# Kernel tuning notes

Measured on AMD Instinct MI355X. Metric: run time of the kernel, lower is better.

## Reference

```python
import jax, jax.numpy as jnp
import numpy as np
import math

D_MODEL = 1024
NHEAD = 16
HEAD_DIM = D_MODEL // NHEAD  # 64
FREQ = 10000.0


def _rope(x, freq=FREQ):
    # x: [B, H, S, D] with D even. Matches RotaryEmbedding.apply:
    # thetas = exp(-2*log(freq)*(i//2)/D) for i in [0, D/2)
    S, D = x.shape[-2], x.shape[-1]
    pos = jnp.arange(S, dtype=x.dtype)                       # [S]
    idx = jnp.arange(D // 2) // 2                            # floor(i/2)
    thetas = jnp.exp((-2.0 * math.log(freq) / D) * idx.astype(x.dtype))  # [D/2]
    ang = pos[:, None] * thetas[None, :]                     # [S, D/2]
    cos, sin = jnp.cos(ang), jnp.sin(ang)
    x2 = x.reshape(*x.shape[:-1], D // 2, 2)
    x0, x1 = x2[..., 0], x2[..., 1]
    out = jnp.stack([x0 * cos - x1 * sin, x0 * sin + x1 * cos], axis=-1)
    return out.reshape(x.shape)


def setup_inputs() -> dict:
    key = jax.random.key(0)
    k1, k2, k3, k4, k5 = jax.random.split(key, 5)
    B, S = 2, 2048
    scale = 1.0 / math.sqrt(D_MODEL)
    return {
        "embeddings": jax.random.normal(k1, (B, S, D_MODEL), dtype=jnp.float32),
        "W_qkv": jax.random.normal(k2, (D_MODEL, 3 * D_MODEL), dtype=jnp.float32) * scale,
        "b_qkv": jnp.zeros((3 * D_MODEL,), dtype=jnp.float32),
        "W_o": jax.random.normal(k4, (D_MODEL, D_MODEL), dtype=jnp.float32) * scale,
        "b_o": jnp.zeros((D_MODEL,), dtype=jnp.float32),
    }


def reference(embeddings, W_qkv, b_qkv, W_o, b_o):
    B, S, _ = embeddings.shape
    qkv = embeddings @ W_qkv + b_qkv                          # [B,S,3*D]
    q, k, v = jnp.split(qkv, 3, axis=-1)

    def split_heads(t):  # [B,S,D] -> [B,H,S,hd]
        return t.reshape(B, S, NHEAD, HEAD_DIM).transpose(0, 2, 1, 3)

    q, k, v = split_heads(q), split_heads(k), split_heads(v)
    q = _rope(q)
    k = _rope(k)

    scores = jnp.einsum("bhqd,bhkd->bhqk", q, k) / math.sqrt(HEAD_DIM)
    attn = jax.nn.softmax(scores, axis=-1)
    heads = jnp.einsum("bhqk,bhkd->bhqd", attn, v)            # [B,H,S,hd]
    out = heads.transpose(0, 2, 1, 3).reshape(B, S, D_MODEL)
    return out @ W_o + b_o
```

## Files before the change

kernel.cpp:

```cpp
#include <hip/hip_runtime.h>
#include <hip/hip_bf16.h>
#include <math.h>

typedef __bf16 bf16;
typedef __bf16 bf16x4 __attribute__((ext_vector_type(4)));
typedef __bf16 bf16x8 __attribute__((ext_vector_type(8)));
typedef float f32x4 __attribute__((ext_vector_type(4)));

#define DEV static __device__ __forceinline__

#define SS 2048
#define HH 16
#define HD 64

DEV void load_lds16(const bf16* g, bf16* l) {
  __builtin_amdgcn_global_load_lds(
      (const __attribute__((address_space(1))) unsigned int*)g,
      (__attribute__((address_space(3))) unsigned int*)l, 16, 0, 0);
}

__global__ __launch_bounds__(256) void k_prep(
    const float* __restrict__ emb, bf16* __restrict__ Xb,
    const float* __restrict__ Wqkv, bf16* __restrict__ Wqt,
    const float* __restrict__ Wo, bf16* __restrict__ Wot) {
  __shared__ float tt[32][33];
  int bid = blockIdx.x;
  if (bid < 4096) {
    int i = (bid * 256 + threadIdx.x) * 4;
    float4 v = *reinterpret_cast<const float4*>(emb + i);
    bf16x4 o = {(bf16)v.x, (bf16)v.y, (bf16)v.z, (bf16)v.w};
    *reinterpret_cast<bf16x4*>(Xb + i) = o;
    return;
  }
  const float* in;
  bf16* out;
  int R = 1024, C, ctile, rtile;
  if (bid < 7168) {
    in = Wqkv; out = Wqt; C = 3072;
    int idx = bid - 4096; ctile = idx % 96; rtile = idx / 96;
  } else {
    in = Wo; out = Wot; C = 1024;
    int idx = bid - 7168; ctile = idx & 31; rtile = idx >> 5;
  }
  int tx = threadIdx.x & 31, ty = threadIdx.x >> 5;
#pragma unroll
  for (int i = 0; i < 4; ++i)
    tt[ty + 8 * i][tx] = in[(rtile * 32 + ty + 8 * i) * C + ctile * 32 + tx];
  __syncthreads();
#pragma unroll
  for (int i = 0; i < 4; ++i) {
    int oc = ctile * 32 + ty + 8 * i;
    out[oc * R + rtile * 32 + tx] = (bf16)tt[tx][ty + 8 * i];
  }
}

DEV void gemm_core(const bf16* __restrict__ Ab, const bf16* __restrict__ Bb,
                   bf16* As, bf16* Bs, int w, int l, f32x4 acc[4][4]) {
  int fr = l & 15, fg = l >> 4;
  int wr = (w >> 1) * 64, wc = (w & 1) * 64;
  for (int kt = 0; kt < 16; ++kt) {
#pragma unroll
    for (int i = 0; i < 4; ++i) {
      int blk = w * 4 + i;
      const bf16* ga = Ab + (blk * 8 + (l >> 3)) * 1024 + kt * 64 + (l & 7) * 8;
      const bf16* gb = Bb + (blk * 8 + (l >> 3)) * 1024 + kt * 64 + (l & 7) * 8;
      load_lds16(ga, As + blk * 512);
      load_lds16(gb, Bs + blk * 512);
    }
    __syncthreads();
#pragma unroll
    for (int kk = 0; kk < 2; ++kk) {
      bf16x8 af[4], bfv[4];
#pragma unroll
      for (int mi = 0; mi < 4; ++mi)
        af[mi] = *(const bf16x8*)(As + (wr + mi * 16 + fr) * 64 + kk * 32 + fg * 8);
#pragma unroll
      for (int ni = 0; ni < 4; ++ni)
        bfv[ni] = *(const bf16x8*)(Bs + (wc + ni * 16 + fr) * 64 + kk * 32 + fg * 8);
#pragma unroll
      for (int mi = 0; mi < 4; ++mi)
#pragma unroll
        for (int ni = 0; ni < 4; ++ni)
          acc[mi][ni] = __builtin_amdgcn_mfma_f32_16x16x32_bf16(
              af[mi], bfv[ni], acc[mi][ni], 0, 0, 0);
    }
    __syncthreads();
  }
}

__global__ __launch_bounds__(256) void k_gemm1(
    const bf16* __restrict__ A, const bf16* __restrict__ Bt,
    const float* __restrict__ bias, bf16* __restrict__ Qo,
    bf16* __restrict__ Ko, bf16* __restrict__ Vo) {
  __shared__ bf16 As[128 * 64], Bs[128 * 64];
  int wg = blockIdx.x;
  int bm = wg & 31, bn = wg >> 5;
  int t = threadIdx.x, w = t >> 6, l = t & 63;
  f32x4 acc[4][4];
#pragma unroll
  for (int mi = 0; mi < 4; ++mi)
#pragma unroll
    for (int ni = 0; ni < 4; ++ni) acc[mi][ni] = (f32x4){0.f, 0.f, 0.f, 0.f};
  gemm_core(A + bm * 128 * 1024, Bt + bn * 128 * 1024, As, Bs, w, l, acc);
  int fr = l & 15, fg = l >> 4;
  int wr = (w >> 1) * 64, wc = (w & 1) * 64;
#pragma unroll
  for (int mi = 0; mi < 4; ++mi)
#pragma unroll
    for (int ni = 0; ni < 4; ++ni) {
      int gc = bn * 128 + wc + ni * 16 + fr;
      int sec = gc >> 10, cc = gc & 1023;
      bf16* dst = sec == 0 ? Qo : (sec == 1 ? Ko : Vo);
      int h = cc >> 6, d = cc & 63;
      float bb = bias[gc];
      int gr0 = bm * 128 + wr + mi * 16 + fg * 4;
#pragma unroll
      for (int r = 0; r < 4; ++r) {
        int gr = gr0 + r;
        int b = gr >> 11, s = gr & 2047;
        dst[((b * HH + h) * SS + s) * HD + d] = (bf16)(acc[mi][ni][r] + bb);
      }
    }
}

__global__ __launch_bounds__(256) void k_gemm2(
    const bf16* __restrict__ A, const bf16* __restrict__ Bt,
    const float* __restrict__ bias, float* __restrict__ out) {
  __shared__ bf16 As[128 * 64], Bs[128 * 64];
  int wg = blockIdx.x;
  int bm = wg & 31, bn = wg >> 5;
  int t = threadIdx.x, w = t >> 6, l = t & 63;
  f32x4 acc[4][4];
#pragma unroll
  for (int mi = 0; mi < 4; ++mi)
#pragma unroll
    for (int ni = 0; ni < 4; ++ni) acc[mi][ni] = (f32x4){0.f, 0.f, 0.f, 0.f};
  gemm_core(A + bm * 128 * 1024, Bt + bn * 128 * 1024, As, Bs, w, l, acc);
  int fr = l & 15, fg = l >> 4;
  int wr = (w >> 1) * 64, wc = (w & 1) * 64;
#pragma unroll
  for (int mi = 0; mi < 4; ++mi)
#pragma unroll
    for (int ni = 0; ni < 4; ++ni) {
      int gc = bn * 128 + wc + ni * 16 + fr;
      float bb = bias[gc];
      int gr0 = bm * 128 + wr + mi * 16 + fg * 4;
#pragma unroll
      for (int r = 0; r < 4; ++r)
        out[(gr0 + r) * 1024 + gc] = acc[mi][ni][r] + bb;
    }
}

__global__ void k_rope(bf16* __restrict__ Qb, bf16* __restrict__ Kb) {
  int t = blockIdx.x * 256 + threadIdx.x;
  bf16* buf = (t >> 19) ? Kb : Qb;
  float qs = (t >> 19) ? 1.0f : 0.125f;
  int g = t & 524287;
  int j = g & 7;
  int s = (g >> 3) & 2047;
  bf16* p = buf + (long long)g * 8;
  const float CN = -0.28782313662425572f;
  float th0 = __expf(CN * (float)(2 * j));
  float th1 = __expf(CN * (float)(2 * j + 1));
  float sp = (float)s;
  float s0, c0, s1, c1;
  sincosf(sp * th0, &s0, &c0);
  sincosf(sp * th1, &s1, &c1);
  bf16x8 v = *(bf16x8*)p;
  float x[8];
#pragma unroll
  for (int i = 0; i < 8; ++i) x[i] = (float)v[i];
  float o[8];
  o[0] = x[0] * c0 - x[1] * s0; o[1] = x[0] * s0 + x[1] * c0;
  o[2] = x[2] * c0 - x[3] * s0; o[3] = x[2] * s0 + x[3] * c0;
  o[4] = x[4] * c1 - x[5] * s1; o[5] = x[4] * s1 + x[5] * c1;
  o[6] = x[6] * c1 - x[7] * s1; o[7] = x[6] * s1 + x[7] * c1;
  bf16x8 ov;
#pragma unroll
  for (int i = 0; i < 8; ++i) ov[i] = (bf16)(o[i] * qs);
  *(bf16x8*)p = ov;
}

__global__ void k_trV(const bf16* __restrict__ V, bf16* __restrict__ Vt) {
  __shared__ bf16 t[64][66];
  int st = blockIdx.x, bh = blockIdx.y;
  const bf16* vb = V + (long long)bh * SS * HD;
  bf16* ob = Vt + (long long)bh * HD * SS;
  int tx = threadIdx.x & 63, ty = threadIdx.x >> 6;
#pragma unroll
  for (int i = 0; i < 16; ++i)
    t[ty + 4 * i][tx] = vb[(st * 64 + ty + 4 * i) * 64 + tx];
  __syncthreads();
#pragma unroll
  for (int i = 0; i < 16; ++i) {
    int dR = ty + 4 * i;
    ob[dR * SS + st * 64 + tx] = t[tx][dR];
  }
}

#define MFMA(a, b, c) __builtin_amdgcn_mfma_f32_16x16x32_bf16(a, b, c, 0, 0, 0)

__global__ __launch_bounds__(512) void k_attn(
    const bf16* __restrict__ Q, const bf16* __restrict__ K,
    const bf16* __restrict__ Vt, bf16* __restrict__ Hd) {
  __shared__ bf16 KVs[2][8192];
  __shared__ bf16 plds[8][16][72];
  int bid = blockIdx.x;
  int x = bid & 7, rr = bid >> 3;
  int bh = x * 4 + (rr & 3);
  int qt = rr >> 2;
  int b = bh >> 4, h = bh & 15;
  int t = threadIdx.x, w = t >> 6, l = t & 63;
  int fr = l & 15, fg = l >> 4;
  const bf16* Qb = Q + (long long)bh * SS * HD;
  const bf16* Kb = K + (long long)bh * SS * HD;
  const bf16* Vb = Vt + (long long)bh * HD * SS;
  bool isK = w < 4;
  int stride = isK ? 64 : 2048;
  int wrow = (isK ? w : (w - 4)) * 16 + (l >> 3);
  const bf16* src = (isK ? Kb : Vb) + wrow * stride + ((l & 7) ^ (l >> 3)) * 8;
  int adv = isK ? 4096 : 64;
  int dbase = w * 1024;

  int q0 = qt * 128 + w * 16;
  bf16x8 qf0 = *(const bf16x8*)(Qb + (q0 + fr) * 64 + fg * 8);
  bf16x8 qf1 = *(const bf16x8*)(Qb + (q0 + fr) * 64 + 32 + fg * 8);
  f32x4 acc[4];
#pragma unroll
  for (int db = 0; db < 4; ++db) acc[db] = (f32x4){0.f, 0.f, 0.f, 0.f};
  float ssum = 0.f;
  const f32x4 zero = {0.f, 0.f, 0.f, 0.f};
  int xo = fr & 7;

  load_lds16(src, &KVs[0][dbase]);
  load_lds16(src + 8 * stride, &KVs[0][dbase + 512]);
  src += adv;
  __syncthreads();

  for (int it = 0; it < 32; ++it) {
    int buf = it & 1;
    if (it < 31) {
      load_lds16(src, &KVs[buf ^ 1][dbase]);
      load_lds16(src + 8 * stride, &KVs[buf ^ 1][dbase + 512]);
      src += adv;
    }
    const bf16* Ks = &KVs[buf][0];
    const bf16* Vs = &KVs[buf][4096];
    f32x4 stl[4];
    __builtin_amdgcn_s_setprio(1);
#pragma unroll
    for (int ks = 0; ks < 4; ++ks) {
      bf16x8 k0 = *(const bf16x8*)(Ks + (ks * 16 + fr) * 64 + (fg ^ xo) * 8);
      bf16x8 k1 = *(const bf16x8*)(Ks + (ks * 16 + fr) * 64 + ((4 + fg) ^ xo) * 8);
      stl[ks] = MFMA(k0, qf0, zero);
      stl[ks] = MFMA(k1, qf1, stl[ks]);
    }
    __builtin_amdgcn_s_setprio(0);
    float ps = 0.f;
#pragma unroll
    for (int ks = 0; ks < 4; ++ks) {
      bf16x4 pb;
#pragma unroll
      for (int r = 0; r < 4; ++r) {
        float p = __expf(stl[ks][r] - 16.0f);
        ps += p;
        pb[r] = (bf16)p;
      }
      *(bf16x4*)&plds[w][fr][ks * 16 + fg * 4] = pb;
    }
    ssum += ps;
    bf16x8 pf0 = *(const bf16x8*)&plds[w][fr][fg * 8];
    bf16x8 pf1 = *(const bf16x8*)&plds[w][fr][32 + fg * 8];
    __builtin_amdgcn_s_setprio(1);
#pragma unroll
    for (int db = 0; db < 4; ++db) {
      bf16x8 vf0 = *(const bf16x8*)(Vs + (db * 16 + fr) * 64 + (fg ^ xo) * 8);
      bf16x8 vf1 = *(const bf16x8*)(Vs + (db * 16 + fr) * 64 + ((4 + fg) ^ xo) * 8);
      acc[db] = MFMA(vf0, pf0, acc[db]);
      acc[db] = MFMA(vf1, pf1, acc[db]);
    }
    __builtin_amdgcn_s_setprio(0);
    __syncthreads();
  }
  float sv = ssum;
  sv += __shfl_xor(sv, 16);
  sv += __shfl_xor(sv, 32);
  float inv = 1.0f / sv;
  int s = q0 + fr;
#pragma unroll
  for (int db = 0; db < 4; ++db) {
    bf16x4 ob;
#pragma unroll
    for (int r = 0; r < 4; ++r) ob[r] = (bf16)(acc[db][r] * inv);
    *(bf16x4*)(Hd + ((long long)(b * SS + s)) * 1024 + h * 64 + db * 16 + fg * 4) = ob;
  }
}

extern "C" void kernel_launch(void* const* d_in, const int* in_sizes, int n_in,
                              void* d_out, int out_size, void* d_ws, size_t ws_size,
                              hipStream_t stream) {
  const float* emb = (const float*)d_in[0];
  const float* Wqkv = (const float*)d_in[1];
  const float* bqkv = (const float*)d_in[2];
  const float* Wo = (const float*)d_in[3];
  const float* bo = (const float*)d_in[4];
  float* out = (float*)d_out;
  char* ws = (char*)d_ws;
  bf16* Xb  = (bf16*)(ws);
  bf16* Wqt = (bf16*)(ws + 8388608);
  bf16* Wot = (bf16*)(ws + 14680064);
  bf16* Qb  = (bf16*)(ws + 16777216);
  bf16* Kb  = (bf16*)(ws + 25165824);
  bf16* Vb  = (bf16*)(ws + 33554432);
  bf16* Vt  = (bf16*)(ws + 41943040);
  bf16* Hd  = (bf16*)(ws + 50331648);

  hipLaunchKernelGGL(k_prep, dim3(8192), dim3(256), 0, stream, emb, Xb, Wqkv, Wqt, Wo, Wot);
  hipLaunchKernelGGL(k_gemm1, dim3(768), dim3(256), 0, stream, Xb, Wqt, bqkv, Qb, Kb, Vb);
  hipLaunchKernelGGL(k_rope, dim3(4096), dim3(256), 0, stream, Qb, Kb);
  hipLaunchKernelGGL(k_trV, dim3(32, 32), dim3(256), 0, stream, Vb, Vt);
  hipLaunchKernelGGL(k_attn, dim3(512), dim3(512), 0, stream, Qb, Kb, Vt, Hd);
  hipLaunchKernelGGL(k_gemm2, dim3(256), dim3(256), 0, stream, Hd, Wot, bo, out);
}
```

Baseline: 143.8 us.

## Rewrite QKV GEMM with 256x256 tiles, double-buffered LDS, and swizzle

The QKV projection GEMM now uses 256x256 output tiles with 512 threads (8 waves, each computing 128x64), so the grid shrinks from 768 to 192 workgroups. Global-to-LDS loads for the next k-tile are issued in chunks between MFMA groups into a double buffer, which leaves one barrier per iteration. The LDS layout uses an XOR swizzle to avoid bank conflicts, MFMA sections are wrapped in s_setprio, and workgroups are remapped across XCDs for cache locality. The intent is more operand reuse and overlap of loads with compute. In exchange it uses 128KB of LDS and many accumulator registers, and with only 192 workgroups it runs one wave of workgroups on fewer CUs than the GPU has.

Result: faster. 138.4 us (-3.7%).

```diff
diff --git a/kernel.cpp b/kernel.cpp
--- a/kernel.cpp
+++ b/kernel.cpp
@@ -18,6 +18,8 @@
       (const __attribute__((address_space(1))) unsigned int*)g,
       (__attribute__((address_space(3))) unsigned int*)l, 16, 0, 0);
 }
+
+#define MFMA(a, b, c) __builtin_amdgcn_mfma_f32_16x16x32_bf16(a, b, c, 0, 0, 0)
 
 __global__ __launch_bounds__(256) void k_prep(
     const float* __restrict__ emb, bf16* __restrict__ Xb,
@@ -54,6 +56,128 @@
   }
 }
 
+__global__ __launch_bounds__(512) void k_gemm1(
+    const bf16* __restrict__ A, const bf16* __restrict__ Bt,
+    const float* __restrict__ bias, bf16* __restrict__ Qo,
+    bf16* __restrict__ Ko, bf16* __restrict__ Vo) {
+  __shared__ bf16 As[2][16384];
+  __shared__ bf16 Bs[2][16384];
+  int wg = blockIdx.x;
+  int xcd = wg & 7, idx = wg >> 3;
+  int wgid = xcd * 24 + idx;
+  int bm = wgid & 15, bn = wgid >> 4;
+  int t = threadIdx.x, w = t >> 6, l = t & 63;
+  int wm = w >> 2, wn = w & 3;
+  int fr = l & 15, fg = l >> 4;
+  const bf16* Ab = A + bm * 256 * 1024;
+  const bf16* Bb = Bt + bn * 256 * 1024;
+  int trow = t >> 3;
+  const bf16* sA = Ab + trow * 1024 + (((t & 7) ^ (trow & 7)) * 8);
+  const bf16* sB = Bb + trow * 1024 + (((t & 7) ^ (trow & 7)) * 8);
+  int dst0 = (w << 9);
+#pragma unroll
+  for (int j = 0; j < 4; ++j) {
+    load_lds16(sA + j * 65536, &As[0][j * 4096 + dst0]);
+    load_lds16(sB + j * 65536, &Bs[0][j * 4096 + dst0]);
+  }
+  f32x4 acc[8][4];
+#pragma unroll
+  for (int mi = 0; mi < 8; ++mi)
+#pragma unroll
+    for (int ni = 0; ni < 4; ++ni) acc[mi][ni] = (f32x4){0.f, 0.f, 0.f, 0.f};
+  int xo = fr & 7;
+  __syncthreads();
+  for (int kt = 0; kt < 16; ++kt) {
+    const bf16* Asb = &As[kt & 1][0];
+    const bf16* Bsb = &Bs[kt & 1][0];
+    bf16* An = &As[(kt & 1) ^ 1][0];
+    bf16* Bn = &Bs[(kt & 1) ^ 1][0];
+    bool st = kt < 15;
+    int ko = (kt + 1) * 64;
+    bf16x8 av[4], bv[4];
+    if (st) {
+      load_lds16(sA + ko, &An[dst0]);
+      load_lds16(sA + 65536 + ko, &An[4096 + dst0]);
+    }
+#pragma unroll
+    for (int ni = 0; ni < 4; ++ni)
+      bv[ni] = *(const bf16x8*)(Bsb + (wn * 64 + ni * 16 + fr) * 64 + (fg ^ xo) * 8);
+#pragma unroll
+    for (int mi = 0; mi < 4; ++mi)
+      av[mi] = *(const bf16x8*)(Asb + (wm * 128 + mi * 16 + fr) * 64 + (fg ^ xo) * 8);
+    __builtin_amdgcn_s_setprio(1);
+#pragma unroll
+    for (int mi = 0; mi < 4; ++mi)
+#pragma unroll
+      for (int ni = 0; ni < 4; ++ni)
+        acc[mi][ni] = MFMA(av[mi], bv[ni], acc[mi][ni]);
+    __builtin_amdgcn_s_setprio(0);
+    if (st) {
+      load_lds16(sA + 131072 + ko, &An[8192 + dst0]);
+      load_lds16(sA + 196608 + ko, &An[12288 + dst0]);
+    }
+#pragma unroll
+    for (int mi = 0; mi < 4; ++mi)
+      av[mi] = *(const bf16x8*)(Asb + (wm * 128 + (mi + 4) * 16 + fr) * 64 + (fg ^ xo) * 8);
+    __builtin_amdgcn_s_setprio(1);
+#pragma unroll
+    for (int mi = 0; mi < 4; ++mi)
+#pragma unroll
+      for (int ni = 0; ni < 4; ++ni)
+        acc[mi + 4][ni] = MFMA(av[mi], bv[ni], acc[mi + 4][ni]);
+    __builtin_amdgcn_s_setprio(0);
+    if (st) {
+      load_lds16(sB + ko, &Bn[dst0]);
+      load_lds16(sB + 65536 + ko, &Bn[4096 + dst0]);
+    }
+#pragma unroll
+    for (int ni = 0; ni < 4; ++ni)
+      bv[ni] = *(const bf16x8*)(Bsb + (wn * 64 + ni * 16 + fr) * 64 + ((4 + fg) ^ xo) * 8);
+#pragma unroll
+    for (int mi = 0; mi < 4; ++mi)
+      av[mi] = *(const bf16x8*)(Asb + (wm * 128 + mi * 16 + fr) * 64 + ((4 + fg) ^ xo) * 8);
+    __builtin_amdgcn_s_setprio(1);
+#pragma unroll
+    for (int mi = 0; mi < 4; ++mi)
+#pragma unroll
+      for (int ni = 0; ni < 4; ++ni)
+        acc[mi][ni] = MFMA(av[mi], bv[ni], acc[mi][ni]);
+    __builtin_amdgcn_s_setprio(0);
+    if (st) {
+      load_lds16(sB + 131072 + ko, &Bn[8192 + dst0]);
+      load_lds16(sB + 196608 + ko, &Bn[12288 + dst0]);
+    }
+#pragma unroll
+    for (int mi = 0; mi < 4; ++mi)
+      av[mi] = *(const bf16x8*)(Asb + (wm * 128 + (mi + 4) * 16 + fr) * 64 + ((4 + fg) ^ xo) * 8);
+    __builtin_amdgcn_s_setprio(1);
+#pragma unroll
+    for (int mi = 0; mi < 4; ++mi)
+#pragma unroll
+      for (int ni = 0; ni < 4; ++ni)
+        acc[mi + 4][ni] = MFMA(av[mi], bv[ni], acc[mi + 4][ni]);
+    __builtin_amdgcn_s_setprio(0);
+    __syncthreads();
+  }
+#pragma unroll
+  for (int mi = 0; mi < 8; ++mi)
+#pragma unroll
+    for (int ni = 0; ni < 4; ++ni) {
+      int gc = bn * 256 + wn * 64 + ni * 16 + fr;
+      int sec = gc >> 10, cc = gc & 1023;
+      bf16* dst = sec == 0 ? Qo : (sec == 1 ? Ko : Vo);
+      int h = cc >> 6, d = cc & 63;
+      float bb = bias[gc];
+      int gr0 = bm * 256 + wm * 128 + mi * 16 + fg * 4;
+#pragma unroll
+      for (int r = 0; r < 4; ++r) {
+        int gr = gr0 + r;
+        int b = gr >> 11, s = gr & 2047;
+        dst[((b * HH + h) * SS + s) * HD + d] = (bf16)(acc[mi][ni][r] + bb);
+      }
+    }
+}
+
 DEV void gemm_core(const bf16* __restrict__ Ab, const bf16* __restrict__ Bb,
                    bf16* As, bf16* Bs, int w, int l, f32x4 acc[4][4]) {
   int fr = l & 15, fg = l >> 4;
@@ -86,41 +210,6 @@
     }
     __syncthreads();
   }
-}
-
-__global__ __launch_bounds__(256) void k_gemm1(
-    const bf16* __restrict__ A, const bf16* __restrict__ Bt,
-    const float* __restrict__ bias, bf16* __restrict__ Qo,
-    bf16* __restrict__ Ko, bf16* __restrict__ Vo) {
-  __shared__ bf16 As[128 * 64], Bs[128 * 64];
-  int wg = blockIdx.x;
-  int bm = wg & 31, bn = wg >> 5;
-  int t = threadIdx.x, w = t >> 6, l = t & 63;
-  f32x4 acc[4][4];
-#pragma unroll
-  for (int mi = 0; mi < 4; ++mi)
-#pragma unroll
-    for (int ni = 0; ni < 4; ++ni) acc[mi][ni] = (f32x4){0.f, 0.f, 0.f, 0.f};
-  gemm_core(A + bm * 128 * 1024, Bt + bn * 128 * 1024, As, Bs, w, l, acc);
-  int fr = l & 15, fg = l >> 4;
-  int wr = (w >> 1) * 64, wc = (w & 1) * 64;
-#pragma unroll
-  for (int mi = 0; mi < 4; ++mi)
-#pragma unroll
-    for (int ni = 0; ni < 4; ++ni) {
-      int gc = bn * 128 + wc + ni * 16 + fr;
-      int sec = gc >> 10, cc = gc & 1023;
-      bf16* dst = sec == 0 ? Qo : (sec == 1 ? Ko : Vo);
-      int h = cc >> 6, d = cc & 63;
-      float bb = bias[gc];
-      int gr0 = bm * 128 + wr + mi * 16 + fg * 4;
-#pragma unroll
-      for (int r = 0; r < 4; ++r) {
-        int gr = gr0 + r;
-        int b = gr >> 11, s = gr & 2047;
-        dst[((b * HH + h) * SS + s) * HD + d] = (bf16)(acc[mi][ni][r] + bb);
-      }
-    }
 }
 
 __global__ __launch_bounds__(256) void k_gemm2(
@@ -197,8 +286,6 @@
     ob[dR * SS + st * 64 + tx] = t[tx][dR];
   }
 }
-
-#define MFMA(a, b, c) __builtin_amdgcn_mfma_f32_16x16x32_bf16(a, b, c, 0, 0, 0)
 
 __global__ __launch_bounds__(512) void k_attn(
     const bf16* __restrict__ Q, const bf16* __restrict__ K,
@@ -316,7 +403,7 @@
   bf16* Hd  = (bf16*)(ws + 50331648);
 
   hipLaunchKernelGGL(k_prep, dim3(8192), dim3(256), 0, stream, emb, Xb, Wqkv, Wqt, Wo, Wot);
-  hipLaunchKernelGGL(k_gemm1, dim3(768), dim3(256), 0, stream, Xb, Wqt, bqkv, Qb, Kb, Vb);
+  hipLaunchKernelGGL(k_gemm1, dim3(192), dim3(512), 0, stream, Xb, Wqt, bqkv, Qb, Kb, Vb);
   hipLaunchKernelGGL(k_rope, dim3(4096), dim3(256), 0, stream, Qb, Kb);
   hipLaunchKernelGGL(k_trV, dim3(32, 32), dim3(256), 0, stream, Vb, Vt);
   hipLaunchKernelGGL(k_attn, dim3(512), dim3(512), 0, stream, Qb, Kb, Vt, Hd);
```

## Rewrite QKV GEMM with 256x256 tiles, double-buffered LDS, XOR swizzle

Applied to the files above, without the earlier changes.

Replaces the 128x128 QKV projection GEMM with a 512-thread 256x256 tile kernel. It double-buffers LDS so global-to-LDS loads overlap the MFMA work, XOR-swizzles LDS to avoid bank conflicts, sets wave priority around the MFMA blocks, and remaps block indices so each XCD handles a group of neighbouring tiles. The larger tile raises operand reuse, but the grid shrinks to 192 blocks on a 256-CU device, which leaves some CUs idle and raises register pressure from 32 accumulators per lane.

New measurement: 132.8 us. 7.6% less time.

```diff
diff --git a/kernel.cpp b/kernel.cpp
--- a/kernel.cpp
+++ b/kernel.cpp
@@ -18,6 +18,8 @@
       (const __attribute__((address_space(1))) unsigned int*)g,
       (__attribute__((address_space(3))) unsigned int*)l, 16, 0, 0);
 }
+
+#define MFMA(a, b, c) __builtin_amdgcn_mfma_f32_16x16x32_bf16(a, b, c, 0, 0, 0)
 
 __global__ __launch_bounds__(256) void k_prep(
     const float* __restrict__ emb, bf16* __restrict__ Xb,
@@ -54,6 +56,106 @@
   }
 }
 
+__global__ __launch_bounds__(512) void k_gemm1(
+    const bf16* __restrict__ A, const bf16* __restrict__ Bt,
+    const float* __restrict__ bias, bf16* __restrict__ Qo,
+    bf16* __restrict__ Ko, bf16* __restrict__ Vo) {
+  __shared__ bf16 As[2][16384];
+  __shared__ bf16 Bs[2][16384];
+  int wg = blockIdx.x;
+  int xcd = wg & 7, idx = wg >> 3;
+  int bm = (xcd & 3) * 4 + (idx & 3);
+  int bn = (xcd >> 2) * 6 + (idx >> 2);
+  int t = threadIdx.x, w = t >> 6, l = t & 63;
+  int wm = w >> 2, wn = w & 3;
+  int fr = l & 15, fg = l >> 4;
+  const bf16* Ab = A + bm * 256 * 1024;
+  const bf16* Bb = Bt + bn * 256 * 1024;
+  int trow = t >> 3;
+  const bf16* sA = Ab + trow * 1024 + (((t & 7) ^ (trow & 7)) * 8);
+  const bf16* sB = Bb + trow * 1024 + (((t & 7) ^ (trow & 7)) * 8);
+  int dst0 = (w << 9);
+  int xo = fr & 7;
+
+#define G1_STAGE(buf, ko)                                         \
+  do {                                                            \
+    _Pragma("unroll")                                             \
+    for (int j = 0; j < 4; ++j) {                                 \
+      load_lds16(sA + j * 65536 + (ko), &As[buf][j * 4096 + dst0]); \
+      load_lds16(sB + j * 65536 + (ko), &Bs[buf][j * 4096 + dst0]); \
+    }                                                             \
+  } while (0)
+
+  f32x4 acc[8][4];
+#pragma unroll
+  for (int mi = 0; mi < 8; ++mi)
+#pragma unroll
+    for (int ni = 0; ni < 4; ++ni) acc[mi][ni] = (f32x4){0.f, 0.f, 0.f, 0.f};
+
+  G1_STAGE(0, 0);
+  asm volatile("s_waitcnt vmcnt(0)" ::: "memory");
+  __builtin_amdgcn_s_barrier();
+
+  for (int kt = 0; kt < 16; ++kt) {
+    int p = kt & 1;
+    const bf16* Asb = &As[p][0];
+    const bf16* Bsb = &Bs[p][0];
+    if (kt < 15) G1_STAGE(p ^ 1, (kt + 1) * 64);
+    bf16x8 av[8], bv[4];
+#pragma unroll
+    for (int ni = 0; ni < 4; ++ni)
+      bv[ni] = *(const bf16x8*)(Bsb + (wn * 64 + ni * 16 + fr) * 64 + (fg ^ xo) * 8);
+#pragma unroll
+    for (int mi = 0; mi < 8; ++mi)
+      av[mi] = *(const bf16x8*)(Asb + (wm * 128 + mi * 16 + fr) * 64 + (fg ^ xo) * 8);
+    asm volatile("s_waitcnt lgkmcnt(0)" ::: "memory");
+    __builtin_amdgcn_sched_barrier(0);
+    __builtin_amdgcn_s_setprio(1);
+#pragma unroll
+    for (int mi = 0; mi < 8; ++mi)
+#pragma unroll
+      for (int ni = 0; ni < 4; ++ni)
+        acc[mi][ni] = MFMA(av[mi], bv[ni], acc[mi][ni]);
+    __builtin_amdgcn_s_setprio(0);
+#pragma unroll
+    for (int ni = 0; ni < 4; ++ni)
+      bv[ni] = *(const bf16x8*)(Bsb + (wn * 64 + ni * 16 + fr) * 64 + ((4 + fg) ^ xo) * 8);
+#pragma unroll
+    for (int mi = 0; mi < 8; ++mi)
+      av[mi] = *(const bf16x8*)(Asb + (wm * 128 + mi * 16 + fr) * 64 + ((4 + fg) ^ xo) * 8);
+    asm volatile("s_waitcnt lgkmcnt(0)" ::: "memory");
+    __builtin_amdgcn_sched_barrier(0);
+    __builtin_amdgcn_s_setprio(1);
+#pragma unroll
+    for (int mi = 0; mi < 8; ++mi)
+#pragma unroll
+      for (int ni = 0; ni < 4; ++ni)
+        acc[mi][ni] = MFMA(av[mi], bv[ni], acc[mi][ni]);
+    __builtin_amdgcn_s_setprio(0);
+    asm volatile("s_waitcnt vmcnt(0)" ::: "memory");
+    __builtin_amdgcn_sched_barrier(0);
+    __builtin_amdgcn_s_barrier();
+  }
+#pragma unroll
+  for (int mi = 0; mi < 8; ++mi)
+#pragma unroll
+    for (int ni = 0; ni < 4; ++ni) {
+      int gc = bn * 256 + wn * 64 + ni * 16 + fr;
+      int sec = gc >> 10, cc = gc & 1023;
+      bf16* dst = sec == 0 ? Qo : (sec == 1 ? Ko : Vo);
+      int h = cc >> 6, d = cc & 63;
+      float bb = bias[gc];
+      int gr0 = bm * 256 + wm * 128 + mi * 16 + fg * 4;
+#pragma unroll
+      for (int r = 0; r < 4; ++r) {
+        int gr = gr0 + r;
+        int b = gr >> 11, s = gr & 2047;
+        dst[((b * HH + h) * SS + s) * HD + d] = (bf16)(acc[mi][ni][r] + bb);
+      }
+    }
+#undef G1_STAGE
+}
+
 DEV void gemm_core(const bf16* __restrict__ Ab, const bf16* __restrict__ Bb,
                    bf16* As, bf16* Bs, int w, int l, f32x4 acc[4][4]) {
   int fr = l & 15, fg = l >> 4;
@@ -86,41 +188,6 @@
     }
     __syncthreads();
   }
-}
-
-__global__ __launch_bounds__(256) void k_gemm1(
-    const bf16* __restrict__ A, const bf16* __restrict__ Bt,
-    const float* __restrict__ bias, bf16* __restrict__ Qo,
-    bf16* __restrict__ Ko, bf16* __restrict__ Vo) {
-  __shared__ bf16 As[128 * 64], Bs[128 * 64];
-  int wg = blockIdx.x;
-  int bm = wg & 31, bn = wg >> 5;
-  int t = threadIdx.x, w = t >> 6, l = t & 63;
-  f32x4 acc[4][4];
-#pragma unroll
-  for (int mi = 0; mi < 4; ++mi)
-#pragma unroll
-    for (int ni = 0; ni < 4; ++ni) acc[mi][ni] = (f32x4){0.f, 0.f, 0.f, 0.f};
-  gemm_core(A + bm * 128 * 1024, Bt + bn * 128 * 1024, As, Bs, w, l, acc);
-  int fr = l & 15, fg = l >> 4;
-  int wr = (w >> 1) * 64, wc = (w & 1) * 64;
-#pragma unroll
-  for (int mi = 0; mi < 4; ++mi)
-#pragma unroll
-    for (int ni = 0; ni < 4; ++ni) {
-      int gc = bn * 128 + wc + ni * 16 + fr;
-      int sec = gc >> 10, cc = gc & 1023;
-      bf16* dst = sec == 0 ? Qo : (sec == 1 ? Ko : Vo);
-      int h = cc >> 6, d = cc & 63;
-      float bb = bias[gc];
-      int gr0 = bm * 128 + wr + mi * 16 + fg * 4;
-#pragma unroll
-      for (int r = 0; r < 4; ++r) {
-        int gr = gr0 + r;
-        int b = gr >> 11, s = gr & 2047;
-        dst[((b * HH + h) * SS + s) * HD + d] = (bf16)(acc[mi][ni][r] + bb);
-      }
-    }
 }
 
 __global__ __launch_bounds__(256) void k_gemm2(
@@ -197,8 +264,6 @@
     ob[dR * SS + st * 64 + tx] = t[tx][dR];
   }
 }
-
-#define MFMA(a, b, c) __builtin_amdgcn_mfma_f32_16x16x32_bf16(a, b, c, 0, 0, 0)
 
 __global__ __launch_bounds__(512) void k_attn(
     const bf16* __restrict__ Q, const bf16* __restrict__ K,
@@ -316,7 +381,7 @@
   bf16* Hd  = (bf16*)(ws + 50331648);
 
   hipLaunchKernelGGL(k_prep, dim3(8192), dim3(256), 0, stream, emb, Xb, Wqkv, Wqt, Wo, Wot);
-  hipLaunchKernelGGL(k_gemm1, dim3(768), dim3(256), 0, stream, Xb, Wqt, bqkv, Qb, Kb, Vb);
+  hipLaunchKernelGGL(k_gemm1, dim3(192), dim3(512), 0, stream, Xb, Wqt, bqkv, Qb, Kb, Vb);
   hipLaunchKernelGGL(k_rope, dim3(4096), dim3(256), 0, stream, Qb, Kb);
   hipLaunchKernelGGL(k_trV, dim3(32, 32), dim3(256), 0, stream, Vb, Vt);
   hipLaunchKernelGGL(k_attn, dim3(512), dim3(512), 0, stream, Qb, Kb, Vt, Hd);
```
